# Kernel optimization log

Measured on AMD Instinct MI355X. Metric: run time of the kernel, lower is better.

Reference implementation:

```python
import jax, jax.numpy as jnp
import numpy as np

T, B = 512, 512          # time steps, batch
F, G = 128, 12           # alphabet/feature size, n genres
H, D1 = 768, 512         # lstm hidden, MLP hidden
A = 128                  # alphabet size (output)


def setup_inputs() -> dict:
    key = jax.random.key(0)
    ks = jax.random.split(key, 14)
    s = 0.05
    inp = {
        "x": jax.random.normal(ks[0], (T, B, F + G), dtype=jnp.float32),
        # LSTMCell 1: input F -> hidden H (gate order i,f,g,o as in torch)
        "W_ih1": jax.random.normal(ks[1], (4 * H, F), dtype=jnp.float32) * s,
        "W_hh1": jax.random.normal(ks[2], (4 * H, H), dtype=jnp.float32) * s,
        "b_ih1": jax.random.normal(ks[3], (4 * H,), dtype=jnp.float32) * s,
        "b_hh1": jax.random.normal(ks[4], (4 * H,), dtype=jnp.float32) * s,
        # LSTMCell 2: input H -> hidden H
        "W_ih2": jax.random.normal(ks[5], (4 * H, H), dtype=jnp.float32) * s,
        "W_hh2": jax.random.normal(ks[6], (4 * H, H), dtype=jnp.float32) * s,
        "b_ih2": jax.random.normal(ks[7], (4 * H,), dtype=jnp.float32) * s,
        "b_hh2": jax.random.normal(ks[8], (4 * H,), dtype=jnp.float32) * s,
        # MLP head: Linear(H+G, 512) -> SELU -> Linear(512, A)
        "l1_w": jax.random.normal(ks[9], (D1, H + G), dtype=jnp.float32) * s,
        "l1_b": jax.random.normal(ks[10], (D1,), dtype=jnp.float32) * s,
        "l2_w": jax.random.normal(ks[11], (A, D1), dtype=jnp.float32) * s,
        "l2_b": jax.random.normal(ks[12], (A,), dtype=jnp.float32) * s,
        "predict": 0,
    }
    return inp


def _lstm_cell(x, h, c, Wi, Wh, bi, bh):
    gates = x @ Wi.T + bi + h @ Wh.T + bh          # [B, 4H]
    i, f, g, o = jnp.split(gates, 4, axis=1)
    c = jax.nn.sigmoid(f) * c + jax.nn.sigmoid(i) * jnp.tanh(g)
    h = jax.nn.sigmoid(o) * jnp.tanh(c)
    return h, c


def reference(x, W_ih1, W_hh1, b_ih1, b_hh1, W_ih2, W_hh2, b_ih2, b_hh2,
              l1_w, l1_b, l2_w, l2_b, predict):
    # predict==0: training-mode forward (no sampling branch). Dropout in eval = identity.
    nB = x.shape[1]
    nG = G
    h0 = jnp.zeros((nB, H), dtype=jnp.float32)
    init = (h0, h0, h0, h0)  # h_t, c_t, h2_t, c2_t

    def step(carry, xt):
        h, c, h2, c2 = carry
        xi = xt[:, :-nG]        # [B, F] character features
        gen = xt[:, -nG:]       # [B, G] genre features
        h, c = _lstm_cell(xi, h, c, W_ih1, W_hh1, b_ih1, b_hh1)
        h2, c2 = _lstm_cell(h, h2, c2, W_ih2, W_hh2, b_ih2, b_hh2)
        z = jnp.concatenate([h2, gen], axis=1)          # [B, H+G]
        out = jax.nn.selu(z @ l1_w.T + l1_b) @ l2_w.T + l2_b  # [B, A]
        return (h, c, h2, c2), out

    _, outputs = jax.lax.scan(step, init, x)   # [T, B, A]
    return outputs
```

## Files before the change

### kernel.cpp

```cpp
#include <hip/hip_runtime.h>

#define Tn 512
#define Bn 512
#define Fn 128
#define Gn 12
#define Hn 768
#define XW 140
#define D1n 512
#define An 128
#define NT 512
#define NB 256
#define NMEM 16
#define MROWS 32
#define UPM 48

#define XOFF 0
#define HOFF 16384
#define LBOFF 114688
#define AGOFF 122880
#define SMEM_BYTES 155648

using bfrag  = __attribute__((ext_vector_type(8))) short;
using f32x4  = __attribute__((ext_vector_type(4))) float;
using short8 = __attribute__((ext_vector_type(8))) short;
using short4v= __attribute__((ext_vector_type(4))) short;
using float4v= __attribute__((ext_vector_type(4))) float;

static const size_t HSTR = (size_t)Bn * Hn;

__device__ __forceinline__ unsigned short f2bf(float x) {
  union { float f; unsigned int u; } v; v.f = x;
  unsigned int r = v.u + 0x7FFFu + ((v.u >> 16) & 1u);
  return (unsigned short)(r >> 16);
}
__device__ __forceinline__ float bf2f(unsigned short h) {
  union { unsigned int u; float f; } v; v.u = ((unsigned int)h) << 16; return v.f;
}
__device__ __forceinline__ float sigmoid_f(float x) { return 1.f / (1.f + __expf(-x)); }
__device__ __forceinline__ float tanh_f(float x) {
  x = fminf(fmaxf(x, -15.f), 15.f);
  float e = __expf(2.f * x);
  return (e - 1.f) / (e + 1.f);
}
__device__ __forceinline__ f32x4 MFMA(bfrag a, bfrag b, f32x4 c) {
  return __builtin_amdgcn_mfma_f32_16x16x32_bf16(a, b, c, 0, 0, 0);
}

__device__ __forceinline__ void ld16llc(uint4& d, const void* p) {
  asm volatile("global_load_dwordx4 %0, %1, off sc0 sc1" : "=&v"(d) : "v"(p));
}
__device__ __forceinline__ void st8llc(void* p, short4v v) {
  unsigned long long u;
  __builtin_memcpy(&u, &v, 8);
  asm volatile("global_store_dwordx2 %0, %1, off sc0 sc1" :: "v"(p), "v"(u) : "memory");
}
__device__ __forceinline__ void vmwait0() {
  asm volatile("s_waitcnt vmcnt(0)" ::: "memory");
  __builtin_amdgcn_sched_barrier(0);
}

__device__ __forceinline__ void group_bar(int* flags, int fbase, int member, int target) {
  vmwait0();
  __syncthreads();
  if (threadIdx.x == 0) {
    __hip_atomic_store(flags + (size_t)(fbase + member) * 32, target,
                       __ATOMIC_RELAXED, __HIP_MEMORY_SCOPE_SYSTEM);
  }
  if (threadIdx.x < NMEM) {
    while (__hip_atomic_load(flags + (size_t)(fbase + threadIdx.x) * 32,
                             __ATOMIC_RELAXED, __HIP_MEMORY_SCOPE_SYSTEM) < target)
      __builtin_amdgcn_s_sleep(1);
  }
  __syncthreads();
}

struct SetupP {
  const float *Wih1f, *Whh1f, *Wih2f, *Whh2f, *l1wf, *l2wf, *bih1, *bhh1, *bih2, *bhh2;
  unsigned short *Wih1, *Whh1, *Wih2, *Whh2, *l1wb, *l2wb;
  float *b1s, *b2s;
  unsigned short *h1, *h2;
  int* flags;
};

__global__ void setup_kernel(SetupP sp) {
  const size_t gtid = (size_t)blockIdx.x * blockDim.x + threadIdx.x;
  const size_t gs = (size_t)gridDim.x * blockDim.x;
  for (size_t i = gtid; i < 3072u*128u; i += gs) sp.Wih1[i] = f2bf(sp.Wih1f[i]);
  for (size_t i = gtid; i < 3072u*768u; i += gs) sp.Whh1[i] = f2bf(sp.Whh1f[i]);
  for (size_t i = gtid; i < 3072u*768u; i += gs) sp.Wih2[i] = f2bf(sp.Wih2f[i]);
  for (size_t i = gtid; i < 3072u*768u; i += gs) sp.Whh2[i] = f2bf(sp.Whh2f[i]);
  for (size_t i = gtid; i < 512u*768u; i += gs) {
    size_t c = i / 768u, k = i - c * 768u;
    sp.l1wb[i] = f2bf(sp.l1wf[c * 780u + k]);
  }
  for (size_t i = gtid; i < 128u*512u; i += gs) sp.l2wb[i] = f2bf(sp.l2wf[i]);
  for (size_t i = gtid; i < 3072u; i += gs) {
    sp.b1s[i] = sp.bih1[i] + sp.bhh1[i];
    sp.b2s[i] = sp.bih2[i] + sp.bhh2[i];
  }
  for (size_t i = gtid; i < 4u*HSTR; i += gs) { sp.h1[i] = 0; sp.h2[i] = 0; }
  for (size_t i = gtid; i < 8192u; i += gs) sp.flags[i] = 0;
}

struct MainP {
  const float* x;
  const float *l1w_f, *l1b, *l2b;
  const unsigned short *Wih1, *Whh1, *Wih2, *Whh2, *l1wb, *l2wb;
  const float *b1s, *b2s;
  unsigned short *h1, *h2, *a1hi;
  float *out;
  int* flags;
};

__device__ __forceinline__ void stage_x(const MainP& P, char* smem, int t, int grow0, int tid) {
  int r = tid >> 4, c0 = (tid & 15) * 8;
  const float* xp = P.x + ((size_t)t * Bn + grow0 + r) * XW + c0;
  float4v v0 = *(const float4v*)xp;
  float4v v1 = *(const float4v*)(xp + 4);
  short8 hv, lv;
  #pragma unroll
  for (int j = 0; j < 4; ++j) {
    unsigned short h = f2bf(v0[j]); hv[j] = (short)h; lv[j] = (short)f2bf(v0[j] - bf2f(h));
  }
  #pragma unroll
  for (int j = 0; j < 4; ++j) {
    unsigned short h = f2bf(v1[j]); hv[4+j] = (short)h; lv[4+j] = (short)f2bf(v1[j] - bf2f(h));
  }
  int g = tid & 15;
  int off = r * 256 + ((g ^ (r & 7)) << 4);
  *(short8*)(smem + XOFF + off) = hv;
  *(short8*)(smem + XOFF + 8192 + off) = lv;
}

__device__ __forceinline__ void h_issue(uint4 (&R)[12], const unsigned short* hi,
    const unsigned short* lo, int grow0, int tid) {
  #pragma unroll
  for (int it = 0; it < 12; ++it) {
    int idx = tid + it * NT;
    int hl = (idx >= 3072) ? 1 : 0;
    int i2 = idx - hl * 3072;
    int r = i2 / 96, gq = i2 - r * 96;
    ld16llc(R[it], (hl ? lo : hi) + (size_t)(grow0 + r) * Hn + gq * 8);
  }
}
__device__ __forceinline__ void h_commit(uint4 (&R)[12], char* smem, int tid) {
  #pragma unroll
  for (int it = 0; it < 12; ++it) {
    int idx = tid + it * NT;
    int hl = (idx >= 3072) ? 1 : 0;
    int i2 = idx - hl * 3072;
    int r = i2 / 96, gq = i2 - r * 96;
    *(uint4*)(smem + HOFF + hl * 49152 + r * 1536 + ((gq ^ (r & 7)) << 4)) = R[it];
  }
}

__device__ __forceinline__ void a1_issue(uint4 (&S)[4], const MainP& P, int grow0, int tid) {
  #pragma unroll
  for (int it = 0; it < 4; ++it) {
    int idx = tid + it * NT;
    int r = idx >> 6, gq = idx & 63;
    ld16llc(S[it], P.a1hi + (size_t)(grow0 + r) * D1n + gq * 8);
  }
}
__device__ __forceinline__ void a1_commit(uint4 (&S)[4], char* smem, int tid) {
  #pragma unroll
  for (int it = 0; it < 4; ++it) {
    int idx = tid + it * NT;
    int r = idx >> 6, gq = idx & 63;
    *(uint4*)(smem + AGOFF + r * 1024 + ((gq ^ (r & 7)) << 4)) = S[it];
  }
}

__device__ __forceinline__ void mfma_x4(const char* smem, const unsigned short* bp, int rr, int lk,
                                        f32x4& A0, f32x4& A1, f32x4& A2) {
  const int rsw = rr & 7;
  const char* ax = smem + XOFF + rr * 256;
  #pragma unroll
  for (int kk = 0; kk < 4; ++kk) {
    int kg = kk * 4 + lk;
    int ao = ((kg ^ rsw) << 4);
    bfrag ahi = *(const bfrag*)(ax + ao);
    bfrag alo = *(const bfrag*)(ax + 8192 + ao);
    bfrag b0 = *(const bfrag*)(bp + kk * 32 + lk * 8);
    bfrag b1 = *(const bfrag*)(bp + 16 * Fn + kk * 32 + lk * 8);
    bfrag b2 = *(const bfrag*)(bp + 32 * Fn + kk * 32 + lk * 8);
    A0 = MFMA(ahi, b0, A0); A0 = MFMA(alo, b0, A0);
    A1 = MFMA(ahi, b1, A1); A1 = MFMA(alo, b1, A1);
    A2 = MFMA(ahi, b2, A2); A2 = MFMA(alo, b2, A2);
  }
}

__device__ __forceinline__ void mfma_h24(const char* smem, const unsigned short* bp, int rr, int lk,
                                         f32x4& A0, f32x4& A1, f32x4& A2) {
  const int rsw = rr & 7;
  const char* ah = smem + HOFF + rr * 1536;
  #pragma unroll 6
  for (int kk = 0; kk < 24; ++kk) {
    int kg = kk * 4 + lk;
    int ao = ((kg ^ rsw) << 4);
    bfrag ahi = *(const bfrag*)(ah + ao);
    bfrag alo = *(const bfrag*)(ah + 49152 + ao);
    bfrag b0 = *(const bfrag*)(bp + kk * 32 + lk * 8);
    bfrag b1 = *(const bfrag*)(bp + 16 * Hn + kk * 32 + lk * 8);
    bfrag b2 = *(const bfrag*)(bp + 32 * Hn + kk * 32 + lk * 8);
    A0 = MFMA(ahi, b0, A0); A0 = MFMA(alo, b0, A0);
    A1 = MFMA(ahi, b1, A1); A1 = MFMA(alo, b1, A1);
    A2 = MFMA(ahi, b2, A2); A2 = MFMA(alo, b2, A2);
  }
}

__device__ __forceinline__ void l1_mfma(const MainP& P, char* smem, int m,
                                        int wv, int lr, int lk) {
  int nt = wv & 1, mt = (wv >> 1) & 1, kh = wv >> 2;
  f32x4 acc = {0.f,0.f,0.f,0.f};
  const int rr = mt * 16 + lr;
  const int rsw = rr & 7;
  const char* ah = smem + HOFF + rr * 1536;
  const unsigned short* bp = P.l1wb + (size_t)(m * 32 + nt * 16 + lr) * Hn + kh * 384;
  #pragma unroll 4
  for (int kk = 0; kk < 12; ++kk) {
    int kg = (kh * 12 + kk) * 4 + lk;
    int ao = ((kg ^ rsw) << 4);
    bfrag ahi = *(const bfrag*)(ah + ao);
    bfrag alo = *(const bfrag*)(ah + 49152 + ao);
    bfrag bw = *(const bfrag*)(bp + kk * 32 + lk * 8);
    acc = MFMA(ahi, bw, acc); acc = MFMA(alo, bw, acc);
  }
  float* lb = (float*)(smem + LBOFF);
  #pragma unroll
  for (int j = 0; j < 4; ++j)
    lb[(kh * 32 + mt * 16 + lk * 4 + j) * 32 + nt * 16 + lr] = acc[j];
}

__device__ __forceinline__ void l1_final(const MainP& P, const char* smem, int m,
                                         int grow0, int t1, int tid) {
  if (tid < 256) {
    int r = tid >> 3, cq = tid & 7;
    int cc = m * 32 + cq * 4;
    const float* lb = (const float*)(smem + LBOFF);
    const float* xg = P.x + ((size_t)t1 * Bn + grow0 + r) * XW + Fn;
    float xgv[Gn];
    #pragma unroll
    for (int qq = 0; qq < Gn; ++qq) xgv[qq] = xg[qq];
    short4v hv;
    #pragma unroll
    for (int j = 0; j < 4; ++j) {
      int c = cq * 4 + j;
      float s = lb[r * 32 + c] + lb[1024 + r * 32 + c] + P.l1b[cc + j];
      const float* wg = P.l1w_f + (size_t)(cc + j) * 780 + 768;
      #pragma unroll
      for (int qq = 0; qq < Gn; ++qq) s += xgv[qq] * wg[qq];
      float a = (s > 0.f) ? 1.0507009873554805f * s
                          : 1.7580993408473766f * (__expf(s) - 1.f);
      hv[j] = (short)f2bf(a);
    }
    st8llc(P.a1hi + (size_t)(grow0 + r) * D1n + cc, hv);
  }
}

__device__ __forceinline__ void write_gbuf(char* smem, const f32x4& A0, const f32x4& A1,
                                           const f32x4& A2, int rf, int q, int lr, int lk) {
  float* gb = (float*)(smem + AGOFF);
  int base = (rf * 16 + lk * 4) * 200 + q * 48 + lr;
  #pragma unroll
  for (int j = 0; j < 4; ++j) {
    gb[base + j * 200]      = A0[j];
    gb[base + j * 200 + 16] = A1[j];
    gb[base + j * 200 + 32] = A2[j];
  }
}

__device__ __forceinline__ void cell_do(const char* smem, const float* bsum,
    float4v& creg, unsigned short* hhi, unsigned short* hlo,
    int grow0, int m, int tid) {
  if (tid < 384) {
    const float* gb = (const float*)(smem + AGOFF);
    int r = tid / 12, lu0 = (tid - r * 12) * 4;
    short4v hv, lv; float4v cn4;
    #pragma unroll
    for (int j = 0; j < 4; ++j) {
      int lu = lu0 + j;
      int u = m * UPM + lu;
      float gi = gb[r * 200 + lu]       + bsum[u];
      float gf = gb[r * 200 + 48 + lu]  + bsum[Hn + u];
      float gg = gb[r * 200 + 96 + lu]  + bsum[2 * Hn + u];
      float go = gb[r * 200 + 144 + lu] + bsum[3 * Hn + u];
      float cn = sigmoid_f(gf) * creg[j] + sigmoid_f(gi) * tanh_f(gg);
      float hn = sigmoid_f(go) * tanh_f(cn);
      cn4[j] = cn;
      unsigned short h = f2bf(hn);
      hv[j] = (short)h;
      lv[j] = (short)f2bf(hn - bf2f(h));
    }
    creg = cn4;
    size_t idx = (size_t)(grow0 + r) * Hn + m * UPM + lu0;
    st8llc(hhi + idx, hv);
    st8llc(hlo + idx, lv);
  }
}

__device__ __forceinline__ void p4b_mfma(const MainP& P, const char* smem, int m, int grow0,
                                         int t1, int wv, int lr, int lk) {
  if (m < 8 && wv < 2) {
    f32x4 o = {0.f,0.f,0.f,0.f};
    const unsigned short* bp = P.l2wb + (size_t)(m * 16 + lr) * 512;
    const int rr2 = wv * 16 + lr, rsw = rr2 & 7;
    const char* ab = smem + AGOFF + rr2 * 1024;
    #pragma unroll 4
    for (int kk = 0; kk < 16; ++kk) {
      int kg = kk * 4 + lk;
      bfrag ah = *(const bfrag*)(ab + ((kg ^ rsw) << 4));
      bfrag bw = *(const bfrag*)(bp + kk * 32 + lk * 8);
      o = MFMA(ah, bw, o);
    }
    float bb = P.l2b[m * 16 + lr];
    #pragma unroll
    for (int j = 0; j < 4; ++j)
      P.out[((size_t)t1 * Bn + grow0 + wv * 16 + lk * 4 + j) * An + m * 16 + lr] = o[j] + bb;
  }
}

__global__ __launch_bounds__(NT) void lstm_main(MainP P) {
  extern __shared__ char smem[];
  const int tid = threadIdx.x;
  const int bid = blockIdx.x;
  const int lane = tid & 63;
  const int wv = tid >> 6;
  const int lr = lane & 15;
  const int lk = lane >> 4;
  const int m = bid & 15;
  const int gid = bid >> 4;
  const int grow0 = gid * MROWS;
  const int q = wv & 3, rf = wv >> 2;
  const int rr = rf * 16 + lr;
  const int fbase = gid * NMEM;
  const size_t wr1 = (size_t)(q * Hn + m * UPM + lr);

  float4v c1reg = {0.f,0.f,0.f,0.f}, c2reg = {0.f,0.f,0.f,0.f};

  for (int i = tid; i < 24576; i += NT) ((int*)(smem + HOFF))[i] = 0;
  __syncthreads();

  for (int t = 0; t < Tn; ++t) {
    const int p = t & 1;
    unsigned short* h1hiC = P.h1 + (size_t)((p ^ 1) * 2)     * HSTR;
    unsigned short* h1loC = P.h1 + (size_t)((p ^ 1) * 2 + 1) * HSTR;
    const unsigned short* h2hiP = P.h2 + (size_t)(p * 2)     * HSTR;
    const unsigned short* h2loP = P.h2 + (size_t)(p * 2 + 1) * HSTR;
    unsigned short* h2hiC = P.h2 + (size_t)((p ^ 1) * 2)     * HSTR;
    unsigned short* h2loC = P.h2 + (size_t)((p ^ 1) * 2 + 1) * HSTR;

    const bool doP4 = (t >= 2) && (m < 8);
    uint4 R[12];
    h_issue(R, h2hiP, h2loP, grow0, tid);
    {
      uint4 S[4];
      if (doP4) a1_issue(S, P, grow0, tid);
      stage_x(P, smem, t, grow0, tid);
      __syncthreads();
      if (doP4) { vmwait0(); a1_commit(S, smem, tid); }
    }
    __syncthreads();
    if (t >= 2) p4b_mfma(P, smem, m, grow0, t - 2, wv, lr, lk);
    {
      f32x4 A0 = {0.f,0.f,0.f,0.f}, A1 = A0, A2 = A0;
      mfma_x4(smem, P.Wih1 + wr1 * Fn, rr, lk, A0, A1, A2);
      mfma_h24(smem, P.Whh1 + wr1 * Hn, rr, lk, A0, A1, A2);
      __syncthreads();
      vmwait0();
      h_commit(R, smem, tid);
      write_gbuf(smem, A0, A1, A2, rf, q, lr, lk);
    }
    __syncthreads();
    cell_do(smem, P.b1s, c1reg, h1hiC, h1loC, grow0, m, tid);
    group_bar(P.flags, fbase, m, 2 * t + 1);

    h_issue(R, h1hiC, h1loC, grow0, tid);
    f32x4 A0 = {0.f,0.f,0.f,0.f}, A1 = A0, A2 = A0;
    mfma_h24(smem, P.Whh2 + wr1 * Hn, rr, lk, A0, A1, A2);
    if (t >= 1) l1_mfma(P, smem, m, wv, lr, lk);
    __syncthreads();
    vmwait0();
    h_commit(R, smem, tid);
    __syncthreads();
    mfma_h24(smem, P.Wih2 + wr1 * Hn, rr, lk, A0, A1, A2);
    write_gbuf(smem, A0, A1, A2, rf, q, lr, lk);
    __syncthreads();
    cell_do(smem, P.b2s, c2reg, h2hiC, h2loC, grow0, m, tid);
    if (t >= 1) l1_final(P, smem, m, grow0, t - 1, tid);
    group_bar(P.flags, fbase, m, 2 * t + 2);
  }

  {
    uint4 S[4]; uint4 R[12];
    if (m < 8) a1_issue(S, P, grow0, tid);
    h_issue(R, P.h2, P.h2 + HSTR, grow0, tid);
    vmwait0();
    if (m < 8) a1_commit(S, smem, tid);
    h_commit(R, smem, tid);
  }
  __syncthreads();
  p4b_mfma(P, smem, m, grow0, 510, wv, lr, lk);
  l1_mfma(P, smem, m, wv, lr, lk);
  __syncthreads();
  l1_final(P, smem, m, grow0, 511, tid);
  group_bar(P.flags, fbase, m, 2 * Tn + 1);
  {
    uint4 S[4];
    if (m < 8) { a1_issue(S, P, grow0, tid); vmwait0(); a1_commit(S, smem, tid); }
  }
  __syncthreads();
  p4b_mfma(P, smem, m, grow0, 511, wv, lr, lk);
}

extern "C" void kernel_launch(void* const* d_in, const int* in_sizes, int n_in,
                              void* d_out, int out_size, void* d_ws, size_t ws_size,
                              hipStream_t stream) {
  const float* x     = (const float*)d_in[0];
  const float* Wih1f = (const float*)d_in[1];
  const float* Whh1f = (const float*)d_in[2];
  const float* bih1  = (const float*)d_in[3];
  const float* bhh1  = (const float*)d_in[4];
  const float* Wih2f = (const float*)d_in[5];
  const float* Whh2f = (const float*)d_in[6];
  const float* bih2  = (const float*)d_in[7];
  const float* bhh2  = (const float*)d_in[8];
  const float* l1wf  = (const float*)d_in[9];
  const float* l1b   = (const float*)d_in[10];
  const float* l2wf  = (const float*)d_in[11];
  const float* l2b   = (const float*)d_in[12];

  char* ws = (char*)d_ws;
  constexpr size_t o_Wih1 = 0;
  constexpr size_t o_Whh1 = o_Wih1 + (size_t)3072 * 128 * 2;
  constexpr size_t o_Wih2 = o_Whh1 + (size_t)3072 * 768 * 2;
  constexpr size_t o_Whh2 = o_Wih2 + (size_t)3072 * 768 * 2;
  constexpr size_t o_l1wb = o_Whh2 + (size_t)3072 * 768 * 2;
  constexpr size_t o_l2wb = o_l1wb + (size_t)512 * 768 * 2;
  constexpr size_t o_b1s  = o_l2wb + (size_t)128 * 512 * 2;
  constexpr size_t o_b2s  = o_b1s + (size_t)3072 * 4;
  constexpr size_t o_h1   = o_b2s + (size_t)3072 * 4;
  constexpr size_t o_h2   = o_h1 + (size_t)4 * 512 * 768 * 2;
  constexpr size_t o_a1hi = o_h2 + (size_t)4 * 512 * 768 * 2;
  constexpr size_t o_flg  = o_a1hi + (size_t)512 * 512 * 2;

  SetupP sp;
  sp.Wih1f = Wih1f; sp.Whh1f = Whh1f; sp.Wih2f = Wih2f; sp.Whh2f = Whh2f;
  sp.l1wf = l1wf; sp.l2wf = l2wf; sp.bih1 = bih1; sp.bhh1 = bhh1; sp.bih2 = bih2; sp.bhh2 = bhh2;
  sp.Wih1 = (unsigned short*)(ws + o_Wih1);
  sp.Whh1 = (unsigned short*)(ws + o_Whh1);
  sp.Wih2 = (unsigned short*)(ws + o_Wih2);
  sp.Whh2 = (unsigned short*)(ws + o_Whh2);
  sp.l1wb = (unsigned short*)(ws + o_l1wb);
  sp.l2wb = (unsigned short*)(ws + o_l2wb);
  sp.b1s  = (float*)(ws + o_b1s);
  sp.b2s  = (float*)(ws + o_b2s);
  sp.h1   = (unsigned short*)(ws + o_h1);
  sp.h2   = (unsigned short*)(ws + o_h2);
  sp.flags = (int*)(ws + o_flg);
  setup_kernel<<<2048, 256, 0, stream>>>(sp);

  MainP mp;
  mp.x = x; mp.l1w_f = l1wf; mp.l1b = l1b; mp.l2b = l2b;
  mp.Wih1 = sp.Wih1; mp.Whh1 = sp.Whh1; mp.Wih2 = sp.Wih2; mp.Whh2 = sp.Whh2;
  mp.l1wb = sp.l1wb; mp.l2wb = sp.l2wb;
  mp.b1s = sp.b1s; mp.b2s = sp.b2s;
  mp.h1 = sp.h1; mp.h2 = sp.h2;
  mp.a1hi = (unsigned short*)(ws + o_a1hi);
  mp.out  = (float*)d_out;
  mp.flags = sp.flags;

  hipFuncSetAttribute((const void*)lstm_main,
                      hipFuncAttributeMaxDynamicSharedMemorySize, SMEM_BYTES);
  lstm_main<<<NB, NT, SMEM_BYTES, stream>>>(mp);
}
```

Measured before the change: 35.06 ms.

## Wavefront-pipeline the two LSTM layers with one barrier per step

```diff
diff --git a/kernel.cpp b/kernel.cpp
--- a/kernel.cpp
+++ b/kernel.cpp
@@ -9,16 +9,16 @@
 #define D1n 512
 #define An 128
 #define NT 512
-#define NB 256
+#define NB 512
 #define NMEM 16
-#define MROWS 32
+#define MROWS 16
 #define UPM 48
 
 #define XOFF 0
-#define HOFF 16384
-#define LBOFF 114688
-#define AGOFF 122880
-#define SMEM_BYTES 155648
+#define HOFF 8192
+#define LBOFF 57344
+#define AGOFF 61440
+#define SMEM_BYTES 77824
 
 using bfrag  = __attribute__((ext_vector_type(8))) short;
 using f32x4  = __attribute__((ext_vector_type(4))) float;
@@ -27,6 +27,7 @@
 using float4v= __attribute__((ext_vector_type(4))) float;
 
 static const size_t HSTR = (size_t)Bn * Hn;
+static const size_t A1SZ = (size_t)Bn * D1n;
 
 __device__ __forceinline__ unsigned short f2bf(float x) {
   union { float f; unsigned int u; } v; v.f = x;
@@ -46,9 +47,6 @@
   return __builtin_amdgcn_mfma_f32_16x16x32_bf16(a, b, c, 0, 0, 0);
 }
 
-__device__ __forceinline__ void ld16llc(uint4& d, const void* p) {
-  asm volatile("global_load_dwordx4 %0, %1, off sc0 sc1" : "=&v"(d) : "v"(p));
-}
 __device__ __forceinline__ void st8llc(void* p, short4v v) {
   unsigned long long u;
   __builtin_memcpy(&u, &v, 8);
@@ -99,7 +97,7 @@
     sp.b2s[i] = sp.bih2[i] + sp.bhh2[i];
   }
   for (size_t i = gtid; i < 4u*HSTR; i += gs) { sp.h1[i] = 0; sp.h2[i] = 0; }
-  for (size_t i = gtid; i < 8192u; i += gs) sp.flags[i] = 0;
+  for (size_t i = gtid; i < 16384u; i += gs) sp.flags[i] = 0;
 }
 
 struct MainP {
@@ -113,74 +111,95 @@
 };
 
 __device__ __forceinline__ void stage_x(const MainP& P, char* smem, int t, int grow0, int tid) {
-  int r = tid >> 4, c0 = (tid & 15) * 8;
-  const float* xp = P.x + ((size_t)t * Bn + grow0 + r) * XW + c0;
-  float4v v0 = *(const float4v*)xp;
-  float4v v1 = *(const float4v*)(xp + 4);
-  short8 hv, lv;
-  #pragma unroll
-  for (int j = 0; j < 4; ++j) {
-    unsigned short h = f2bf(v0[j]); hv[j] = (short)h; lv[j] = (short)f2bf(v0[j] - bf2f(h));
-  }
-  #pragma unroll
-  for (int j = 0; j < 4; ++j) {
-    unsigned short h = f2bf(v1[j]); hv[4+j] = (short)h; lv[4+j] = (short)f2bf(v1[j] - bf2f(h));
-  }
-  int g = tid & 15;
-  int off = r * 256 + ((g ^ (r & 7)) << 4);
-  *(short8*)(smem + XOFF + off) = hv;
-  *(short8*)(smem + XOFF + 8192 + off) = lv;
-}
-
-__device__ __forceinline__ void h_issue(uint4 (&R)[12], const unsigned short* hi,
+  if (tid < 256) {
+    int r = tid >> 4, g = tid & 15;
+    const float* xp = P.x + ((size_t)t * Bn + grow0 + r) * XW + g * 8;
+    float4v v0 = *(const float4v*)xp;
+    float4v v1 = *(const float4v*)(xp + 4);
+    short8 hv, lv;
+    #pragma unroll
+    for (int j = 0; j < 4; ++j) {
+      unsigned short h = f2bf(v0[j]); hv[j] = (short)h; lv[j] = (short)f2bf(v0[j] - bf2f(h));
+    }
+    #pragma unroll
+    for (int j = 0; j < 4; ++j) {
+      unsigned short h = f2bf(v1[j]); hv[4+j] = (short)h; lv[4+j] = (short)f2bf(v1[j] - bf2f(h));
+    }
+    int off = r * 256 + ((g ^ (r & 7)) << 4);
+    *(short8*)(smem + XOFF + off) = hv;
+    *(short8*)(smem + XOFF + 4096 + off) = lv;
+  }
+}
+
+__device__ __forceinline__ void stage_h_fused(char* smem, const unsigned short* hi,
     const unsigned short* lo, int grow0, int tid) {
-  #pragma unroll
-  for (int it = 0; it < 12; ++it) {
-    int idx = tid + it * NT;
-    int hl = (idx >= 3072) ? 1 : 0;
-    int i2 = idx - hl * 3072;
-    int r = i2 / 96, gq = i2 - r * 96;
-    ld16llc(R[it], (hl ? lo : hi) + (size_t)(grow0 + r) * Hn + gq * 8);
-  }
-}
-__device__ __forceinline__ void h_commit(uint4 (&R)[12], char* smem, int tid) {
-  #pragma unroll
-  for (int it = 0; it < 12; ++it) {
-    int idx = tid + it * NT;
-    int hl = (idx >= 3072) ? 1 : 0;
-    int i2 = idx - hl * 3072;
-    int r = i2 / 96, gq = i2 - r * 96;
-    *(uint4*)(smem + HOFF + hl * 49152 + r * 1536 + ((gq ^ (r & 7)) << 4)) = R[it];
-  }
-}
-
-__device__ __forceinline__ void a1_issue(uint4 (&S)[4], const MainP& P, int grow0, int tid) {
-  #pragma unroll
-  for (int it = 0; it < 4; ++it) {
-    int idx = tid + it * NT;
+  const unsigned short *p0,*p1,*p2,*p3,*p4,*p5;
+  int o0,o1,o2,o3,o4,o5;
+#define HADDR(IT, P, O) { \
+    int idx = tid + IT * NT; \
+    int hl = (idx >= 1536) ? 1 : 0; \
+    int i2 = idx - hl * 1536; \
+    int r = i2 / 96, gq = i2 - r * 96; \
+    P = (hl ? lo : hi) + (size_t)(grow0 + r) * Hn + gq * 8; \
+    O = HOFF + hl * 24576 + r * 1536 + ((gq ^ (r & 7)) << 4); }
+  HADDR(0, p0, o0) HADDR(1, p1, o1) HADDR(2, p2, o2)
+  HADDR(3, p3, o3) HADDR(4, p4, o4) HADDR(5, p5, o5)
+#undef HADDR
+  uint4 R0,R1,R2,R3,R4,R5;
+  asm volatile(
+    "global_load_dwordx4 %0, %6, off sc0 sc1\n\t"
+    "global_load_dwordx4 %1, %7, off sc0 sc1\n\t"
+    "global_load_dwordx4 %2, %8, off sc0 sc1\n\t"
+    "global_load_dwordx4 %3, %9, off sc0 sc1\n\t"
+    "global_load_dwordx4 %4, %10, off sc0 sc1\n\t"
+    "global_load_dwordx4 %5, %11, off sc0 sc1\n\t"
+    "s_waitcnt vmcnt(0)"
+    : "=&v"(R0),"=&v"(R1),"=&v"(R2),"=&v"(R3),"=&v"(R4),"=&v"(R5)
+    : "v"(p0),"v"(p1),"v"(p2),"v"(p3),"v"(p4),"v"(p5)
+    : "memory");
+  *(uint4*)(smem + o0) = R0;
+  *(uint4*)(smem + o1) = R1;
+  *(uint4*)(smem + o2) = R2;
+  *(uint4*)(smem + o3) = R3;
+  *(uint4*)(smem + o4) = R4;
+  *(uint4*)(smem + o5) = R5;
+}
+
+__device__ __forceinline__ void stage_a1_fused(char* smem, const unsigned short* a1p,
+                                               int grow0, int tid) {
+  const unsigned short *p0, *p1;
+  int o0, o1;
+  {
+    int r = tid >> 6, gq = tid & 63;
+    p0 = a1p + (size_t)(grow0 + r) * D1n + gq * 8;
+    o0 = AGOFF + r * 1024 + ((gq ^ (r & 7)) << 4);
+  }
+  {
+    int idx = tid + NT;
     int r = idx >> 6, gq = idx & 63;
-    ld16llc(S[it], P.a1hi + (size_t)(grow0 + r) * D1n + gq * 8);
-  }
-}
-__device__ __forceinline__ void a1_commit(uint4 (&S)[4], char* smem, int tid) {
-  #pragma unroll
-  for (int it = 0; it < 4; ++it) {
-    int idx = tid + it * NT;
-    int r = idx >> 6, gq = idx & 63;
-    *(uint4*)(smem + AGOFF + r * 1024 + ((gq ^ (r & 7)) << 4)) = S[it];
-  }
-}
-
-__device__ __forceinline__ void mfma_x4(const char* smem, const unsigned short* bp, int rr, int lk,
+    p1 = a1p + (size_t)(grow0 + r) * D1n + gq * 8;
+    o1 = AGOFF + r * 1024 + ((gq ^ (r & 7)) << 4);
+  }
+  uint4 S0, S1;
+  asm volatile(
+    "global_load_dwordx4 %0, %2, off sc0 sc1\n\t"
+    "global_load_dwordx4 %1, %3, off sc0 sc1\n\t"
+    "s_waitcnt vmcnt(0)"
+    : "=&v"(S0), "=&v"(S1) : "v"(p0), "v"(p1) : "memory");
+  *(uint4*)(smem + o0) = S0;
+  *(uint4*)(smem + o1) = S1;
+}
+
+__device__ __forceinline__ void mfma_x4(const char* smem, const unsigned short* bp, int lr, int lk,
                                         f32x4& A0, f32x4& A1, f32x4& A2) {
-  const int rsw = rr & 7;
-  const char* ax = smem + XOFF + rr * 256;
+  const int rsw = lr & 7;
+  const char* ax = smem + XOFF + lr * 256;
   #pragma unroll
   for (int kk = 0; kk < 4; ++kk) {
     int kg = kk * 4 + lk;
     int ao = ((kg ^ rsw) << 4);
     bfrag ahi = *(const bfrag*)(ax + ao);
-    bfrag alo = *(const bfrag*)(ax + 8192 + ao);
+    bfrag alo = *(const bfrag*)(ax + 4096 + ao);
     bfrag b0 = *(const bfrag*)(bp + kk * 32 + lk * 8);
     bfrag b1 = *(const bfrag*)(bp + 16 * Fn + kk * 32 + lk * 8);
     bfrag b2 = *(const bfrag*)(bp + 32 * Fn + kk * 32 + lk * 8);
@@ -190,16 +209,16 @@
   }
 }
 
-__device__ __forceinline__ void mfma_h24(const char* smem, const unsigned short* bp, int rr, int lk,
+__device__ __forceinline__ void mfma_h24(const char* smem, const unsigned short* bp, int lr, int lk,
                                          f32x4& A0, f32x4& A1, f32x4& A2) {
-  const int rsw = rr & 7;
-  const char* ah = smem + HOFF + rr * 1536;
+  const int rsw = lr & 7;
+  const char* ah = smem + HOFF + lr * 1536;
   #pragma unroll 6
   for (int kk = 0; kk < 24; ++kk) {
     int kg = kk * 4 + lk;
     int ao = ((kg ^ rsw) << 4);
     bfrag ahi = *(const bfrag*)(ah + ao);
-    bfrag alo = *(const bfrag*)(ah + 49152 + ao);
+    bfrag alo = *(const bfrag*)(ah + 24576 + ao);
     bfrag b0 = *(const bfrag*)(bp + kk * 32 + lk * 8);
     bfrag b1 = *(const bfrag*)(bp + 16 * Hn + kk * 32 + lk * 8);
     bfrag b2 = *(const bfrag*)(bp + 32 * Hn + kk * 32 + lk * 8);
@@ -210,32 +229,32 @@
 }
 
 __device__ __forceinline__ void l1_mfma(const MainP& P, char* smem, int m,
-                                        int wv, int lr, int lk) {
-  int nt = wv & 1, mt = (wv >> 1) & 1, kh = wv >> 2;
+                                        int q, int lr, int lk) {
+  int nt = q & 1, kh = q >> 1;
   f32x4 acc = {0.f,0.f,0.f,0.f};
-  const int rr = mt * 16 + lr;
-  const int rsw = rr & 7;
-  const char* ah = smem + HOFF + rr * 1536;
+  const int rsw = lr & 7;
+  const char* ah = smem + HOFF + lr * 1536;
   const unsigned short* bp = P.l1wb + (size_t)(m * 32 + nt * 16 + lr) * Hn + kh * 384;
   #pragma unroll 4
   for (int kk = 0; kk < 12; ++kk) {
     int kg = (kh * 12 + kk) * 4 + lk;
     int ao = ((kg ^ rsw) << 4);
     bfrag ahi = *(const bfrag*)(ah + ao);
-    bfrag alo = *(const bfrag*)(ah + 49152 + ao);
+    bfrag alo = *(const bfrag*)(ah + 24576 + ao);
     bfrag bw = *(const bfrag*)(bp + kk * 32 + lk * 8);
     acc = MFMA(ahi, bw, acc); acc = MFMA(alo, bw, acc);
   }
   float* lb = (float*)(smem + LBOFF);
   #pragma unroll
   for (int j = 0; j < 4; ++j)
-    lb[(kh * 32 + mt * 16 + lk * 4 + j) * 32 + nt * 16 + lr] = acc[j];
+    lb[(kh * 16 + lk * 4 + j) * 32 + nt * 16 + lr] = acc[j];
 }
 
 __device__ __forceinline__ void l1_final(const MainP& P, const char* smem, int m,
                                          int grow0, int t1, int tid) {
-  if (tid < 256) {
-    int r = tid >> 3, cq = tid & 7;
+  if (tid >= 256 && tid < 384) {
+    int idx = tid - 256;
+    int r = idx >> 3, cq = idx & 7;
     int cc = m * 32 + cq * 4;
     const float* lb = (const float*)(smem + LBOFF);
     const float* xg = P.x + ((size_t)t1 * Bn + grow0 + r) * XW + Fn;
@@ -246,7 +265,7 @@
     #pragma unroll
     for (int j = 0; j < 4; ++j) {
       int c = cq * 4 + j;
-      float s = lb[r * 32 + c] + lb[1024 + r * 32 + c] + P.l1b[cc + j];
+      float s = lb[r * 32 + c] + lb[(16 + r) * 32 + c] + P.l1b[cc + j];
       const float* wg = P.l1w_f + (size_t)(cc + j) * 780 + 768;
       #pragma unroll
       for (int qq = 0; qq < Gn; ++qq) s += xgv[qq] * wg[qq];
@@ -254,26 +273,27 @@
                           : 1.7580993408473766f * (__expf(s) - 1.f);
       hv[j] = (short)f2bf(a);
     }
-    st8llc(P.a1hi + (size_t)(grow0 + r) * D1n + cc, hv);
+    unsigned short* a1w = P.a1hi + (size_t)(t1 & 1) * A1SZ;
+    st8llc(a1w + (size_t)(grow0 + r) * D1n + cc, hv);
   }
 }
 
 __device__ __forceinline__ void write_gbuf(char* smem, const f32x4& A0, const f32x4& A1,
-                                           const f32x4& A2, int rf, int q, int lr, int lk) {
+                                           const f32x4& A2, int q, int lr, int lk) {
   float* gb = (float*)(smem + AGOFF);
-  int base = (rf * 16 + lk * 4) * 200 + q * 48 + lr;
+  int base = (q * 16 + lk * 4) * 48 + lr;
   #pragma unroll
   for (int j = 0; j < 4; ++j) {
-    gb[base + j * 200]      = A0[j];
-    gb[base + j * 200 + 16] = A1[j];
-    gb[base + j * 200 + 32] = A2[j];
+    gb[base + j * 48]      = A0[j];
+    gb[base + j * 48 + 16] = A1[j];
+    gb[base + j * 48 + 32] = A2[j];
   }
 }
 
 __device__ __forceinline__ void cell_do(const char* smem, const float* bsum,
     float4v& creg, unsigned short* hhi, unsigned short* hlo,
     int grow0, int m, int tid) {
-  if (tid < 384) {
+  if (tid < 192) {
     const float* gb = (const float*)(smem + AGOFF);
     int r = tid / 12, lu0 = (tid - r * 12) * 4;
     short4v hv, lv; float4v cn4;
@@ -281,10 +301,10 @@
     for (int j = 0; j < 4; ++j) {
       int lu = lu0 + j;
       int u = m * UPM + lu;
-      float gi = gb[r * 200 + lu]       + bsum[u];
-      float gf = gb[r * 200 + 48 + lu]  + bsum[Hn + u];
-      float gg = gb[r * 200 + 96 + lu]  + bsum[2 * Hn + u];
-      float go = gb[r * 200 + 144 + lu] + bsum[3 * Hn + u];
+      float gi = gb[(0*16 + r) * 48 + lu] + bsum[u];
+      float gf = gb[(1*16 + r) * 48 + lu] + bsum[Hn + u];
+      float gg = gb[(2*16 + r) * 48 + lu] + bsum[2 * Hn + u];
+      float go = gb[(3*16 + r) * 48 + lu] + bsum[3 * Hn + u];
       float cn = sigmoid_f(gf) * creg[j] + sigmoid_f(gi) * tanh_f(gg);
       float hn = sigmoid_f(go) * tanh_f(cn);
       cn4[j] = cn;
@@ -300,27 +320,25 @@
 }
 
 __device__ __forceinline__ void p4b_mfma(const MainP& P, const char* smem, int m, int grow0,
-                                         int t1, int wv, int lr, int lk) {
-  if (m < 8 && wv < 2) {
-    f32x4 o = {0.f,0.f,0.f,0.f};
-    const unsigned short* bp = P.l2wb + (size_t)(m * 16 + lr) * 512;
-    const int rr2 = wv * 16 + lr, rsw = rr2 & 7;
-    const char* ab = smem + AGOFF + rr2 * 1024;
-    #pragma unroll 4
-    for (int kk = 0; kk < 16; ++kk) {
-      int kg = kk * 4 + lk;
-      bfrag ah = *(const bfrag*)(ab + ((kg ^ rsw) << 4));
-      bfrag bw = *(const bfrag*)(bp + kk * 32 + lk * 8);
-      o = MFMA(ah, bw, o);
-    }
-    float bb = P.l2b[m * 16 + lr];
-    #pragma unroll
-    for (int j = 0; j < 4; ++j)
-      P.out[((size_t)t1 * Bn + grow0 + wv * 16 + lk * 4 + j) * An + m * 16 + lr] = o[j] + bb;
-  }
-}
-
-__global__ __launch_bounds__(NT) void lstm_main(MainP P) {
+                                         int t1, int lr, int lk) {
+  f32x4 o = {0.f,0.f,0.f,0.f};
+  const unsigned short* bp = P.l2wb + (size_t)(m * 16 + lr) * 512;
+  const int rsw = lr & 7;
+  const char* ab = smem + AGOFF + lr * 1024;
+  #pragma unroll 4
+  for (int kk = 0; kk < 16; ++kk) {
+    int kg = kk * 4 + lk;
+    bfrag ah = *(const bfrag*)(ab + ((kg ^ rsw) << 4));
+    bfrag bw = *(const bfrag*)(bp + kk * 32 + lk * 8);
+    o = MFMA(ah, bw, o);
+  }
+  float bb = P.l2b[m * 16 + lr];
+  #pragma unroll
+  for (int j = 0; j < 4; ++j)
+    P.out[((size_t)t1 * Bn + grow0 + lk * 4 + j) * An + m * 16 + lr] = o[j] + bb;
+}
+
+__global__ __launch_bounds__(NT, 4) void lstm_main(MainP P) {
   extern __shared__ char smem[];
   const int tid = threadIdx.x;
   const int bid = blockIdx.x;
@@ -331,86 +349,72 @@
   const int m = bid & 15;
   const int gid = bid >> 4;
   const int grow0 = gid * MROWS;
-  const int q = wv & 3, rf = wv >> 2;
-  const int rr = rf * 16 + lr;
+  const int q = wv & 3;
+  const int hw = wv >> 2;
   const int fbase = gid * NMEM;
   const size_t wr1 = (size_t)(q * Hn + m * UPM + lr);
 
   float4v c1reg = {0.f,0.f,0.f,0.f}, c2reg = {0.f,0.f,0.f,0.f};
 
-  for (int i = tid; i < 24576; i += NT) ((int*)(smem + HOFF))[i] = 0;
-  __syncthreads();
-
-  for (int t = 0; t < Tn; ++t) {
-    const int p = t & 1;
-    unsigned short* h1hiC = P.h1 + (size_t)((p ^ 1) * 2)     * HSTR;
-    unsigned short* h1loC = P.h1 + (size_t)((p ^ 1) * 2 + 1) * HSTR;
-    const unsigned short* h2hiP = P.h2 + (size_t)(p * 2)     * HSTR;
-    const unsigned short* h2loP = P.h2 + (size_t)(p * 2 + 1) * HSTR;
-    unsigned short* h2hiC = P.h2 + (size_t)((p ^ 1) * 2)     * HSTR;
-    unsigned short* h2loC = P.h2 + (size_t)((p ^ 1) * 2 + 1) * HSTR;
-
-    const bool doP4 = (t >= 2) && (m < 8);
-    uint4 R[12];
-    h_issue(R, h2hiP, h2loP, grow0, tid);
-    {
-      uint4 S[4];
-      if (doP4) a1_issue(S, P, grow0, tid);
-      stage_x(P, smem, t, grow0, tid);
-      __syncthreads();
-      if (doP4) { vmwait0(); a1_commit(S, smem, tid); }
-    }
-    __syncthreads();
-    if (t >= 2) p4b_mfma(P, smem, m, grow0, t - 2, wv, lr, lk);
-    {
-      f32x4 A0 = {0.f,0.f,0.f,0.f}, A1 = A0, A2 = A0;
-      mfma_x4(smem, P.Wih1 + wr1 * Fn, rr, lk, A0, A1, A2);
-      mfma_h24(smem, P.Whh1 + wr1 * Hn, rr, lk, A0, A1, A2);
-      __syncthreads();
-      vmwait0();
-      h_commit(R, smem, tid);
-      write_gbuf(smem, A0, A1, A2, rf, q, lr, lk);
-    }
-    __syncthreads();
-    cell_do(smem, P.b1s, c1reg, h1hiC, h1loC, grow0, m, tid);
-    group_bar(P.flags, fbase, m, 2 * t + 1);
-
-    h_issue(R, h1hiC, h1loC, grow0, tid);
+  for (int t = 0; t <= Tn + 2; ++t) {
+    const int r1 = (t - 1) & 1;
+    const int w1 = t & 1;
+    const int r2 = t & 1;
+    const int w2 = (t - 1) & 1;
+    const unsigned short* h1hiR = P.h1 + (size_t)(r1 * 2)     * HSTR;
+    const unsigned short* h1loR = P.h1 + (size_t)(r1 * 2 + 1) * HSTR;
+    unsigned short* h1hiW = P.h1 + (size_t)(w1 * 2)     * HSTR;
+    unsigned short* h1loW = P.h1 + (size_t)(w1 * 2 + 1) * HSTR;
+    const unsigned short* h2hiR = P.h2 + (size_t)(r2 * 2)     * HSTR;
+    const unsigned short* h2loR = P.h2 + (size_t)(r2 * 2 + 1) * HSTR;
+    unsigned short* h2hiW = P.h2 + (size_t)(w2 * 2)     * HSTR;
+    unsigned short* h2loW = P.h2 + (size_t)(w2 * 2 + 1) * HSTR;
+
+    const bool doG1 = (t < Tn);
+    const bool doH1 = (t <= Tn);
+    const bool doG2 = (t >= 1 && t <= Tn);
+    const bool doH2 = (t >= 1 && t <= Tn + 1);
+    const bool doL1 = (t >= 2 && t <= Tn + 1);
+    const bool doP4 = (t >= 3) && (m < 8);
+
+    if (doG1) stage_x(P, smem, t, grow0, tid);
+    if (doH1) stage_h_fused(smem, h1hiR, h1loR, grow0, tid);
+    if (doP4) stage_a1_fused(smem, P.a1hi + (size_t)((t - 1) & 1) * A1SZ, grow0, tid);
+    __syncthreads();
+
+    if (doP4 && wv == 0) p4b_mfma(P, smem, m, grow0, t - 3, lr, lk);
+
     f32x4 A0 = {0.f,0.f,0.f,0.f}, A1 = A0, A2 = A0;
-    mfma_h24(smem, P.Whh2 + wr1 * Hn, rr, lk, A0, A1, A2);
-    if (t >= 1) l1_mfma(P, smem, m, wv, lr, lk);
-    __syncthreads();
-    vmwait0();
-    h_commit(R, smem, tid);
-    __syncthreads();
-    mfma_h24(smem, P.Wih2 + wr1 * Hn, rr, lk, A0, A1, A2);
-    write_gbuf(smem, A0, A1, A2, rf, q, lr, lk);
-    __syncthreads();
-    cell_do(smem, P.b2s, c2reg, h2hiC, h2loC, grow0, m, tid);
-    if (t >= 1) l1_final(P, smem, m, grow0, t - 1, tid);
-    group_bar(P.flags, fbase, m, 2 * t + 2);
-  }
-
-  {
-    uint4 S[4]; uint4 R[12];
-    if (m < 8) a1_issue(S, P, grow0, tid);
-    h_issue(R, P.h2, P.h2 + HSTR, grow0, tid);
-    vmwait0();
-    if (m < 8) a1_commit(S, smem, tid);
-    h_commit(R, smem, tid);
-  }
-  __syncthreads();
-  p4b_mfma(P, smem, m, grow0, 510, wv, lr, lk);
-  l1_mfma(P, smem, m, wv, lr, lk);
-  __syncthreads();
-  l1_final(P, smem, m, grow0, 511, tid);
-  group_bar(P.flags, fbase, m, 2 * Tn + 1);
-  {
-    uint4 S[4];
-    if (m < 8) { a1_issue(S, P, grow0, tid); vmwait0(); a1_commit(S, smem, tid); }
-  }
-  __syncthreads();
-  p4b_mfma(P, smem, m, grow0, 511, wv, lr, lk);
+    if (hw == 0) {
+      if (doG1) {
+        mfma_x4(smem, P.Wih1 + wr1 * Fn, lr, lk, A0, A1, A2);
+        mfma_h24(smem, P.Whh1 + wr1 * Hn, lr, lk, A0, A1, A2);
+      }
+    } else {
+      if (doG2) mfma_h24(smem, P.Wih2 + wr1 * Hn, lr, lk, A0, A1, A2);
+    }
+    __syncthreads();
+
+    if (doH2) stage_h_fused(smem, h2hiR, h2loR, grow0, tid);
+    __syncthreads();
+
+    if (hw == 0) {
+      if (doL1) l1_mfma(P, smem, m, q, lr, lk);
+    } else {
+      if (doG2) mfma_h24(smem, P.Whh2 + wr1 * Hn, lr, lk, A0, A1, A2);
+    }
+    __syncthreads();
+
+    if (hw == 0 && doG1) write_gbuf(smem, A0, A1, A2, q, lr, lk);
+    __syncthreads();
+    if (doG1) cell_do(smem, P.b1s, c1reg, h1hiW, h1loW, grow0, m, tid);
+    __syncthreads();
+    if (hw == 1 && doG2) write_gbuf(smem, A0, A1, A2, q, lr, lk);
+    __syncthreads();
+    if (doG2) cell_do(smem, P.b2s, c2reg, h2hiW, h2loW, grow0, m, tid);
+    if (doL1) l1_final(P, smem, m, grow0, t - 2, tid);
+    group_bar(P.flags, fbase, m, t + 1);
+  }
 }
 
 extern "C" void kernel_launch(void* const* d_in, const int* in_sizes, int n_in,
@@ -442,7 +446,7 @@
   constexpr size_t o_h1   = o_b2s + (size_t)3072 * 4;
   constexpr size_t o_h2   = o_h1 + (size_t)4 * 512 * 768 * 2;
   constexpr size_t o_a1hi = o_h2 + (size_t)4 * 512 * 768 * 2;
-  constexpr size_t o_flg  = o_a1hi + (size_t)512 * 512 * 2;
+  constexpr size_t o_flg  = o_a1hi + (size_t)2 * 512 * 512 * 2;
 
   SetupP sp;
   sp.Wih1f = Wih1f; sp.Whh1f = Whh1f; sp.Wih2f = Wih2f; sp.Whh2f = Whh2f;
```

Result: faster. 33.64 ms (-4.1%).
